# Optimization experiments

Hardware: AMD Instinct MI355X
Metric: run time of the kernel (lower is better)

Reference implementation:

```python
import jax, jax.numpy as jnp
import numpy as np

UNITS = 512
EPS = 1e-6

def setup_inputs() -> dict:
    key = jax.random.key(0)
    x = jax.random.normal(key, (262144, UNITS), dtype=jnp.float32)
    return {"x": x}

def reference(x):
    d = x.shape[1]
    # Gram matrix with diagonal jitter: [d, d]
    g = x.T @ x + jnp.eye(d, dtype=x.dtype) * EPS
    L = jnp.linalg.cholesky(g)  # lower triangular [d, d]
    # inv(L) via triangular solve (same math as tf.linalg.inv on L)
    L_inv = jax.scipy.linalg.solve_triangular(L, jnp.eye(d, dtype=x.dtype), lower=True)
    ortho_weights = L_inv.T * jnp.sqrt(jnp.float32(UNITS))
    return x @ ortho_weights
```

## Files before the change

kernel.cpp:

```cpp
#include <hip/hip_runtime.h>


#define EPSJ 1e-6f
#define SQRTD 22.627416997969522f

typedef short bf16x8 __attribute__((ext_vector_type(8)));
typedef float f32x4 __attribute__((ext_vector_type(4)));

__device__ __forceinline__ unsigned short f2bf(float f) {
  unsigned u = __float_as_uint(f);
  unsigned r = u + 0x7fffu + ((u >> 16) & 1u);
  return (unsigned short)(r >> 16);
}

__device__ __forceinline__ int swz(int row, int slot) {
  return slot ^ ((row ^ (row >> 3)) & 7);
}

__device__ __forceinline__ float wred(float s) {
  s += __shfl_xor(s, 1);  s += __shfl_xor(s, 2);  s += __shfl_xor(s, 4);
  s += __shfl_xor(s, 8);  s += __shfl_xor(s, 16); s += __shfl_xor(s, 32);
  return s;
}

#define GLOAD16(g, l)                                                         \
  __builtin_amdgcn_global_load_lds(                                           \
      (const __attribute__((address_space(1))) void*)(g),                     \
      (__attribute__((address_space(3))) void*)(l), 16, 0, 0)

__global__ void convert_bf(const float* __restrict__ X,
                           unsigned short* __restrict__ Xbf) {
  long idx = (long)blockIdx.x * blockDim.x + threadIdx.x;
  const long stride = (long)gridDim.x * blockDim.x;
  const long nch = 134217728 / 8;
  for (long i = idx; i < nch; i += stride) {
    float4 f0 = ((const float4*)X)[i * 2];
    float4 f1 = ((const float4*)X)[i * 2 + 1];
    uint4 o;
    o.x = (unsigned)f2bf(f0.x) | ((unsigned)f2bf(f0.y) << 16);
    o.y = (unsigned)f2bf(f0.z) | ((unsigned)f2bf(f0.w) << 16);
    o.z = (unsigned)f2bf(f1.x) | ((unsigned)f2bf(f1.y) << 16);
    o.w = (unsigned)f2bf(f1.z) | ((unsigned)f2bf(f1.w) << 16);
    ((uint4*)Xbf)[i] = o;
  }
}

__device__ __forceinline__ void stage_pack4(
    const unsigned short* __restrict__ src,
    unsigned short* dst, int c0, int kg) {
  uint4 r0 = *(const uint4*)src;
  uint4 r1 = *(const uint4*)(src + 512);
  uint4 r2 = *(const uint4*)(src + 1024);
  uint4 r3 = *(const uint4*)(src + 1536);
  unsigned a[4] = {r0.x, r0.y, r0.z, r0.w};
  unsigned b[4] = {r1.x, r1.y, r1.z, r1.w};
  unsigned c[4] = {r2.x, r2.y, r2.z, r2.w};
  unsigned d[4] = {r3.x, r3.y, r3.z, r3.w};
  const int khi = kg >> 1, koff = (kg & 1) * 8;
  #pragma unroll
  for (int s = 0; s < 8; ++s) {
    int wsel = s >> 1, sh = (s & 1) * 16;
    unsigned v0 = (a[wsel] >> sh) & 0xFFFFu;
    unsigned v1 = (b[wsel] >> sh) & 0xFFFFu;
    unsigned v2 = (c[wsel] >> sh) & 0xFFFFu;
    unsigned v3 = (d[wsel] >> sh) & 0xFFFFu;
    int cc = c0 + s;
    int sl = khi ^ ((cc ^ (cc >> 3)) & 7);
    *(uint2*)((char*)dst + cc * 128 + sl * 16 + koff) =
        make_uint2(v0 | (v1 << 16), v2 | (v3 << 16));
  }
}

__global__ __launch_bounds__(512, 2) void gram_bf(
    const unsigned short* __restrict__ Xbf, float* __restrict__ part,
    int nchunk) {
  __shared__ unsigned short As[256 * 64];
  __shared__ unsigned short Bs[256 * 64];
  const int b = blockIdx.x, pos = b % 3, chunk = b / 3;
  const int s0 = (int)((long)4096 * chunk / nchunk);
  const int s1 = (int)((long)4096 * (chunk + 1) / nchunk);
  const int ca = (pos == 1) ? 256 : 0;
  const int cb2 = (pos == 0) ? 0 : 256;
  const bool diag = (pos != 2);
  const int t = threadIdx.x, lane = t & 63, w = t >> 6;
  const int wr = w >> 2, wc = w & 3;

  f32x4 acc[8][4];
  const f32x4 zf = {0.f, 0.f, 0.f, 0.f};
  #pragma unroll
  for (int a = 0; a < 8; ++a)
    #pragma unroll
    for (int bb = 0; bb < 4; ++bb) acc[a][bb] = zf;

  const int c0 = (t & 31) * 8;
  const int kg = t >> 5;

  for (int ks = s0; ks < s1; ++ks) {
    long r = (long)ks * 64 + kg * 4;
    stage_pack4(Xbf + r * 512 + ca + c0, As, c0, kg);
    if (!diag) stage_pack4(Xbf + r * 512 + cb2 + c0, Bs, c0, kg);
    __syncthreads();
    const unsigned short* Bp = diag ? As : Bs;
    #pragma unroll
    for (int kk = 0; kk < 2; ++kk) {
      bf16x8 af[8], bfr[4];
      #pragma unroll
      for (int fm = 0; fm < 8; ++fm) {
        int row = wr * 128 + fm * 16 + (lane & 15);
        int slot = swz(row, kk * 4 + (lane >> 4));
        af[fm] = *(const bf16x8*)((const char*)As + row * 128 + slot * 16);
      }
      #pragma unroll
      for (int fn = 0; fn < 4; ++fn) {
        int row = wc * 64 + fn * 16 + (lane & 15);
        int slot = swz(row, kk * 4 + (lane >> 4));
        bfr[fn] = *(const bf16x8*)((const char*)Bp + row * 128 + slot * 16);
      }
      #pragma unroll
      for (int fm = 0; fm < 8; ++fm)
        #pragma unroll
        for (int fn = 0; fn < 4; ++fn)
          acc[fm][fn] = __builtin_amdgcn_mfma_f32_16x16x32_bf16(
              bfr[fn], af[fm], acc[fm][fn], 0, 0, 0);
    }
    __syncthreads();
  }
  float* out = part + (long)b * 65536;
  #pragma unroll
  for (int fm = 0; fm < 8; ++fm)
    #pragma unroll
    for (int fn = 0; fn < 4; ++fn) {
      int mi = wr * 128 + fm * 16 + (lane & 15);
      int nj = wc * 64 + fn * 16 + (lane >> 4) * 4;
      *(float4*)(out + mi * 256 + nj) = *(float4*)&acc[fm][fn];
    }
}

__global__ __launch_bounds__(512, 2) void gram_f32(
    const float* __restrict__ X, float* __restrict__ part, int nchunk) {
  __shared__ unsigned short As[256 * 64];
  __shared__ unsigned short Bs[256 * 64];
  const int b = blockIdx.x;
  const int pos = b % 3;
  const int chunk = b / 3;
  const int CR = 262144 / nchunk;
  const long r0 = (long)chunk * CR;
  const int ca = (pos == 1) ? 256 : 0;
  const int cb = (pos == 0) ? 0 : 256;
  const bool diag = (pos != 2);
  const int t = threadIdx.x, lane = t & 63, w = t >> 6;
  const int wr = w >> 2, wc = w & 3;

  f32x4 acc[8][4];
  const f32x4 zf = {0.f, 0.f, 0.f, 0.f};
  #pragma unroll
  for (int a = 0; a < 8; ++a)
    #pragma unroll
    for (int bb = 0; bb < 4; ++bb) acc[a][bb] = zf;

  const int c_oct = t & 31, msub = t >> 5;

  for (int ks = 0; ks < CR; ks += 64) {
    #pragma unroll
    for (int it = 0; it < 4; ++it) {
      int m = msub + 16 * it;
      long row = r0 + ks + m;
      const float4* sa = (const float4*)(X + row * 512 + ca + c_oct * 8);
      float4 a0 = sa[0], a1 = sa[1];
      {
        float v[8] = {a0.x, a0.y, a0.z, a0.w, a1.x, a1.y, a1.z, a1.w};
        #pragma unroll
        for (int s = 0; s < 8; ++s) {
          int c = c_oct * 8 + s;
          int off = c * 128 + ((2 * m) ^ (((c ^ (c >> 3)) & 7) << 4));
          *(unsigned short*)((char*)As + off) = f2bf(v[s]);
        }
      }
      if (!diag) {
        const float4* sb = (const float4*)(X + row * 512 + cb + c_oct * 8);
        float4 b0 = sb[0], b1 = sb[1];
        float v[8] = {b0.x, b0.y, b0.z, b0.w, b1.x, b1.y, b1.z, b1.w};
        #pragma unroll
        for (int s = 0; s < 8; ++s) {
          int c = c_oct * 8 + s;
          int off = c * 128 + ((2 * m) ^ (((c ^ (c >> 3)) & 7) << 4));
          *(unsigned short*)((char*)Bs + off) = f2bf(v[s]);
        }
      }
    }
    __syncthreads();
    const unsigned short* Bp = diag ? As : Bs;
    #pragma unroll
    for (int kk = 0; kk < 2; ++kk) {
      bf16x8 af[8], bfr[4];
      #pragma unroll
      for (int fm = 0; fm < 8; ++fm) {
        int row = wr * 128 + fm * 16 + (lane & 15);
        int slot = swz(row, kk * 4 + (lane >> 4));
        af[fm] = *(const bf16x8*)((const char*)As + row * 128 + slot * 16);
      }
      #pragma unroll
      for (int fn = 0; fn < 4; ++fn) {
        int row = wc * 64 + fn * 16 + (lane & 15);
        int slot = swz(row, kk * 4 + (lane >> 4));
        bfr[fn] = *(const bf16x8*)((const char*)Bp + row * 128 + slot * 16);
      }
      #pragma unroll
      for (int fm = 0; fm < 8; ++fm)
        #pragma unroll
        for (int fn = 0; fn < 4; ++fn)
          acc[fm][fn] = __builtin_amdgcn_mfma_f32_16x16x32_bf16(
              af[fm], bfr[fn], acc[fm][fn], 0, 0, 0);
    }
    __syncthreads();
  }
  float* out = part + (long)b * 65536;
  #pragma unroll
  for (int fm = 0; fm < 8; ++fm)
    #pragma unroll
    for (int fn = 0; fn < 4; ++fn)
      #pragma unroll
      for (int j = 0; j < 4; ++j) {
        int i  = wr * 128 + fm * 16 + (lane >> 4) * 4 + j;
        int jj = wc * 64 + fn * 16 + (lane & 15);
        out[i * 256 + jj] = acc[fm][fn][j];
      }
}

__global__ void gram_reduce(const float* __restrict__ part,
                            float* __restrict__ G, int nchunk) {
  int idx = blockIdx.x * 256 + threadIdx.x;
  int pos = idx >> 16;
  int e = idx & 65535;
  float s = 0.f;
  for (int ch = 0; ch < nchunk; ++ch)
    s += part[(long)(ch * 3 + pos) * 65536 + e];
  int i = e >> 8, j = e & 255;
  if (pos == 0) {
    G[i * 512 + j] = s;
  } else if (pos == 1) {
    G[(256 + i) * 512 + 256 + j] = s;
  } else {
    G[i * 512 + 256 + j] = s;
    G[(256 + j) * 512 + i] = s;
  }
}

__global__ __launch_bounds__(256) void chol_d64(float* __restrict__ G,
                                                float* __restrict__ Dinv,
                                                int p) {
  __shared__ float Pb[64][65];
  __shared__ float Sb[64][65];
  __shared__ float Inv[64][65];
  __shared__ float Tt[32][33];
  const int t = threadIdx.x;
  const int r0 = 64 * p;
  const int tr = (t >> 4) * 4, tc = (t & 15) * 4;

  for (int idx = t; idx < 4096; idx += 256) {
    int i = idx >> 6, j = idx & 63;
    float v = G[(long)(r0 + i) * 512 + r0 + j];
    if (i == j) v += EPSJ;
    Pb[i][j] = v;
  }
  __syncthreads();

  if (p > 0) {
    float cc[4][4] = {{0.f}};
    for (int r = 0; r < p; ++r) {
      for (int idx = t; idx < 4096; idx += 256) {
        int i = idx >> 6, j = idx & 63;
        Sb[i][j] = G[(long)(r0 + i) * 512 + 64 * r + j];
      }
      __syncthreads();
      #pragma unroll 4
      for (int k = 0; k < 64; ++k) {
        float a0 = Sb[tr][k], a1 = Sb[tr+1][k], a2 = Sb[tr+2][k], a3 = Sb[tr+3][k];
        float b0 = Sb[tc][k], b1 = Sb[tc+1][k], b2 = Sb[tc+2][k], b3 = Sb[tc+3][k];
        cc[0][0]+=a0*b0; cc[0][1]+=a0*b1; cc[0][2]+=a0*b2; cc[0][3]+=a0*b3;
        cc[1][0]+=a1*b0; cc[1][1]+=a1*b1; cc[1][2]+=a1*b2; cc[1][3]+=a1*b3;
        cc[2][0]+=a2*b0; cc[2][1]+=a2*b1; cc[2][2]+=a2*b2; cc[2][3]+=a2*b3;
        cc[3][0]+=a3*b0; cc[3][1]+=a3*b1; cc[3][2]+=a3*b2; cc[3][3]+=a3*b3;
      }
      __syncthreads();
    }
    #pragma unroll
    for (int u = 0; u < 4; ++u)
      #pragma unroll
      for (int v = 0; v < 4; ++v)
        Pb[tr + u][tc + v] -= cc[u][v];
    __syncthreads();
  }

  const int lane = t & 63, w = t >> 6;
  #pragma unroll
  for (int sp = 0; sp < 2; ++sp) {
    const int b0 = sp * 32;
    if (w == 0) {
      float rr[32];
      #pragma unroll
      for (int k = 0; k < 32; ++k)
        rr[k] = (lane < 32) ? Pb[b0 + lane][b0 + k] : 0.f;
      #pragma unroll
      for (int j = 0; j < 32; ++j) {
        float d = sqrtf(__shfl(rr[j], j));
        if (lane == j) rr[j] = d;
        else if (lane > j && lane < 32) rr[j] = rr[j] / d;
        float rj = rr[j];
        #pragma unroll
        for (int k = j + 1; k < 32; ++k) {
          float Lkj = __shfl(rj, k);
          if (lane > j && lane < 32) rr[k] -= rj * Lkj;
        }
      }
      #pragma unroll
      for (int k = 0; k < 32; ++k)
        if (lane < 32) Pb[b0 + lane][b0 + k] = rr[k];
    }
    __syncthreads();
    if (sp == 0) {
      if (t < 32) {
        int rw = 32 + t;
        float x[32];
        #pragma unroll
        for (int j = 0; j < 32; ++j) x[j] = Pb[rw][j];
        #pragma unroll
        for (int j = 0; j < 32; ++j) {
          float xj = x[j] / Pb[j][j];
          x[j] = xj;
          #pragma unroll
          for (int k2 = j + 1; k2 < 32; ++k2) x[k2] -= xj * Pb[k2][j];
        }
        #pragma unroll
        for (int j = 0; j < 32; ++j) Pb[rw][j] = x[j];
      }
      __syncthreads();
      {
        int i = 32 + (t >> 3), kb = 32 + (t & 7) * 4;
        float sv[4];
        #pragma unroll
        for (int e = 0; e < 4; ++e) sv[e] = Pb[i][kb + e];
        #pragma unroll 4
        for (int j = 0; j < 32; ++j) {
          float aij = Pb[i][j];
          #pragma unroll
          for (int e = 0; e < 4; ++e) sv[e] -= aij * Pb[kb + e][j];
        }
        #pragma unroll
        for (int e = 0; e < 4; ++e) Pb[i][kb + e] = sv[e];
      }
      __syncthreads();
    }
  }

  if (t < 64) {
    int col = t & 31, o = (t >> 5) * 32;
    float x[32];
    #pragma unroll
    for (int i = 0; i < 32; ++i) {
      float s = (i == col) ? 1.f : 0.f;
      #pragma unroll
      for (int j = 0; j < i; ++j) s -= Pb[o + i][o + j] * x[j];
      x[i] = s / Pb[o + i][o + i];
    }
    #pragma unroll
    for (int i = 0; i < 32; ++i) Inv[o + i][o + col] = x[i];
  }
  for (int idx = t; idx < 1024; idx += 256)
    Inv[idx >> 5][32 + (idx & 31)] = 0.f;
  __syncthreads();
  {
    int i = t >> 3, jb = (t & 7) * 4;
    float sv[4] = {0.f, 0.f, 0.f, 0.f};
    #pragma unroll 4
    for (int k = 0; k < 32; ++k) {
      float bik = Pb[32 + i][k];
      #pragma unroll
      for (int e = 0; e < 4; ++e) sv[e] += bik * Inv[k][jb + e];
    }
    #pragma unroll
    for (int e = 0; e < 4; ++e) Tt[i][jb + e] = sv[e];
  }
  __syncthreads();
  {
    int i = t >> 3, jb = (t & 7) * 4;
    float sv[4] = {0.f, 0.f, 0.f, 0.f};
    #pragma unroll 4
    for (int k = 0; k < 32; ++k) {
      float cik = Inv[32 + i][32 + k];
      #pragma unroll
      for (int e = 0; e < 4; ++e) sv[e] += cik * Tt[k][jb + e];
    }
    #pragma unroll
    for (int e = 0; e < 4; ++e) Inv[32 + i][jb + e] = -sv[e];
  }
  __syncthreads();
  for (int idx = t; idx < 4096; idx += 256) {
    int i = idx >> 6, j = idx & 63;
    G[(long)(r0 + i) * 512 + r0 + j] = Pb[i][j];
    Dinv[p * 4096 + idx] = Inv[i][j];
  }
}

__global__ __launch_bounds__(256) void chol_t64(float* __restrict__ G,
                                                const float* __restrict__ Dinv,
                                                int p) {
  __shared__ float SbI[64][65];
  __shared__ float SbP[64][65];
  __shared__ float Ub[64][65];
  __shared__ float Db[64][65];
  const int t = threadIdx.x;
  const long rI = 64 * (p + 1 + blockIdx.x), cP = 64 * p;
  const int tr = (t >> 4) * 4, tc = (t & 15) * 4;

  for (int idx = t; idx < 4096; idx += 256)
    Db[idx >> 6][idx & 63] = Dinv[p * 4096 + idx];

  float cc[4][4] = {{0.f}};
  for (int r = 0; r < p; ++r) {
    __syncthreads();
    for (int idx = t; idx < 4096; idx += 256) {
      int i = idx >> 6, j = idx & 63;
      SbI[i][j] = G[(rI + i) * 512 + 64 * r + j];
      SbP[i][j] = G[(cP + i) * 512 + 64 * r + j];
    }
    __syncthreads();
    #pragma unroll 4
    for (int k = 0; k < 64; ++k) {
      float a0 = SbI[tr][k], a1 = SbI[tr+1][k], a2 = SbI[tr+2][k], a3 = SbI[tr+3][k];
      float b0 = SbP[tc][k], b1 = SbP[tc+1][k], b2 = SbP[tc+2][k], b3 = SbP[tc+3][k];
      cc[0][0]+=a0*b0; cc[0][1]+=a0*b1; cc[0][2]+=a0*b2; cc[0][3]+=a0*b3;
      cc[1][0]+=a1*b0; cc[1][1]+=a1*b1; cc[1][2]+=a1*b2; cc[1][3]+=a1*b3;
      cc[2][0]+=a2*b0; cc[2][1]+=a2*b1; cc[2][2]+=a2*b2; cc[2][3]+=a2*b3;
      cc[3][0]+=a3*b0; cc[3][1]+=a3*b1; cc[3][2]+=a3*b2; cc[3][3]+=a3*b3;
    }
  }
  __syncthreads();
  #pragma unroll
  for (int u = 0; u < 4; ++u)
    #pragma unroll
    for (int v = 0; v < 4; ++v)
      Ub[tr + u][tc + v] =
          G[(rI + tr + u) * 512 + cP + tc + v] - cc[u][v];
  __syncthreads();
  float xx[4][4] = {{0.f}};
  #pragma unroll 4
  for (int k = 0; k < 64; ++k) {
    float a0 = Ub[tr][k], a1 = Ub[tr+1][k], a2 = Ub[tr+2][k], a3 = Ub[tr+3][k];
    float b0 = Db[tc][k], b1 = Db[tc+1][k], b2 = Db[tc+2][k], b3 = Db[tc+3][k];
    xx[0][0]+=a0*b0; xx[0][1]+=a0*b1; xx[0][2]+=a0*b2; xx[0][3]+=a0*b3;
    xx[1][0]+=a1*b0; xx[1][1]+=a1*b1; xx[1][2]+=a1*b2; xx[1][3]+=a1*b3;
    xx[2][0]+=a2*b0; xx[2][1]+=a2*b1; xx[2][2]+=a2*b2; xx[2][3]+=a2*b3;
    xx[3][0]+=a3*b0; xx[3][1]+=a3*b1; xx[3][2]+=a3*b2; xx[3][3]+=a3*b3;
  }
  #pragma unroll
  for (int u = 0; u < 4; ++u)
    #pragma unroll
    for (int v = 0; v < 4; ++v)
      G[(rI + tr + u) * 512 + cP + tc + v] = xx[u][v];
}

__global__ __launch_bounds__(256) void tri_assemble(
    const float* __restrict__ G, const float* __restrict__ Dinv,
    unsigned short* __restrict__ Wt) {
  __shared__ float Bsh[448 * 64];
  __shared__ float T[64 * 64];
  const int q = blockIdx.x, t = threadIdx.x;
  const int or_ = (t >> 4) * 4, oc = (t & 15) * 4;

  for (int p = q + 1; p < 8; ++p) {
    float cc[4][4] = {{0.f}};
    for (int r = q; r < p; ++r) {
      const float* Lbase = G + (long)(64 * p) * 512 + 64 * r;
      #pragma unroll 4
      for (int k = 0; k < 64; ++k) {
        float a0 = Lbase[(or_ + 0) * 512 + k];
        float a1 = Lbase[(or_ + 1) * 512 + k];
        float a2 = Lbase[(or_ + 2) * 512 + k];
        float a3 = Lbase[(or_ + 3) * 512 + k];
        float b0, b1, b2, b3;
        if (r == q) {
          const float* Bq = Dinv + q * 4096 + k * 64 + oc;
          b0 = Bq[0]; b1 = Bq[1]; b2 = Bq[2]; b3 = Bq[3];
        } else {
          const float* Br = Bsh + ((r - q - 1) * 64 + k) * 64 + oc;
          b0 = Br[0]; b1 = Br[1]; b2 = Br[2]; b3 = Br[3];
        }
        cc[0][0] += a0*b0; cc[0][1] += a0*b1; cc[0][2] += a0*b2; cc[0][3] += a0*b3;
        cc[1][0] += a1*b0; cc[1][1] += a1*b1; cc[1][2] += a1*b2; cc[1][3] += a1*b3;
        cc[2][0] += a2*b0; cc[2][1] += a2*b1; cc[2][2] += a2*b2; cc[2][3] += a2*b3;
        cc[3][0] += a3*b0; cc[3][1] += a3*b1; cc[3][2] += a3*b2; cc[3][3] += a3*b3;
      }
    }
    #pragma unroll
    for (int u = 0; u < 4; ++u)
      #pragma unroll
      for (int v = 0; v < 4; ++v)
        T[(or_ + u) * 64 + oc + v] = cc[u][v];
    __syncthreads();

    float c2[4][4] = {{0.f}};
    const float* Dp = Dinv + p * 4096;
    #pragma unroll 4
    for (int k = 0; k < 64; ++k) {
      float a0 = Dp[(or_ + 0) * 64 + k];
      float a1 = Dp[(or_ + 1) * 64 + k];
      float a2 = Dp[(or_ + 2) * 64 + k];
      float a3 = Dp[(or_ + 3) * 64 + k];
      const float* Tk = T + k * 64 + oc;
      float b0 = Tk[0], b1 = Tk[1], b2 = Tk[2], b3 = Tk[3];
      c2[0][0] += a0*b0; c2[0][1] += a0*b1; c2[0][2] += a0*b2; c2[0][3] += a0*b3;
      c2[1][0] += a1*b0; c2[1][1] += a1*b1; c2[1][2] += a1*b2; c2[1][3] += a1*b3;
      c2[2][0] += a2*b0; c2[2][1] += a2*b1; c2[2][2] += a2*b2; c2[2][3] += a2*b3;
      c2[3][0] += a3*b0; c2[3][1] += a3*b1; c2[3][2] += a3*b2; c2[3][3] += a3*b3;
    }
    #pragma unroll
    for (int u = 0; u < 4; ++u)
      #pragma unroll
      for (int v = 0; v < 4; ++v)
        Bsh[((p - q - 1) * 64 + or_ + u) * 64 + oc + v] = -c2[u][v];
    __syncthreads();
  }

  const int nr = (8 - q) * 64;
  for (int idx = t; idx < nr * 64; idx += 256) {
    int i = idx >> 6, kk = idx & 63;
    float v = (i < 64) ? Dinv[q * 4096 + i * 64 + kk]
                       : Bsh[(i - 64) * 64 + kk];
    int n = 64 * q + i;
    Wt[(long)n * 512 + 64 * q + kk] = f2bf(SQRTD * v);
  }
  for (int idx = t; idx < 64 * q * 64; idx += 256) {
    int n = idx >> 6, kk = idx & 63;
    Wt[(long)n * 512 + 64 * q + kk] = 0;
  }
}

__global__ void tri_inv(const float* __restrict__ G,
                        unsigned short* __restrict__ Wt) {
  int w = threadIdx.x >> 6, lane = threadIdx.x & 63;
  int c = blockIdx.x * 4 + w;
  float v8[8];
  #pragma unroll
  for (int q = 0; q < 8; ++q) v8[q] = 0.f;
  #pragma unroll
  for (int q = 0; q < 8; ++q) {
    for (int ii = 0; ii < 64; ++ii) {
      int i = q * 64 + ii;
      const float* Lrow = G + (long)i * 512;
      float s = 0.f;
      #pragma unroll
      for (int qq = 0; qq < 8; ++qq) {
        if (qq < q) s += v8[qq] * Lrow[qq * 64 + lane];
      }
      s += (lane < ii) ? v8[q] * Lrow[q * 64 + lane] : 0.f;
      s = wred(s);
      float xi = (((i == c) ? 1.f : 0.f) - s) / Lrow[i];
      if (lane == ii) v8[q] = xi;
    }
  }
  #pragma unroll
  for (int q = 0; q < 8; ++q) {
    int i = q * 64 + lane;
    Wt[(long)i * 512 + c] = f2bf(SQRTD * v8[q]);
  }
}

__global__ __launch_bounds__(256, 3) void ymm3(
    const unsigned short* __restrict__ Xbf,
    const unsigned short* __restrict__ Wt, float* __restrict__ Y) {
  __shared__ unsigned short As[2][128 * 64];
  const int t = threadIdx.x, lane = t & 63, w = t >> 6;
  const int id = blockIdx.x;
  const int xcd = id & 7, j = id >> 3;
  const long m0 = (long)((j >> 2) * 8 + xcd) * 128;
  const int n0 = (j & 3) * 128;
  const int wm = (w >> 1) * 64, wn = (w & 1) * 64;
  const int lrow = lane >> 3, lslot = lane & 7;
  f32x4 acc[4][4];
  const f32x4 zf = {0.f, 0.f, 0.f, 0.f};
  #pragma unroll
  for (int a = 0; a < 4; ++a)
    #pragma unroll
    for (int bq = 0; bq < 4; ++bq) acc[a][bq] = zf;

  auto stage = [&](int buf, int k0) {
    #pragma unroll
    for (int jj = 0; jj < 4; ++jj) {
      int row = (w * 4 + jj) * 8 + lrow;
      const unsigned short* sA =
          Xbf + (m0 + row) * 512 + k0 + swz(row, lslot) * 8;
      GLOAD16(sA, &As[buf][(w * 4 + jj) * 512]);
    }
  };

  stage(0, 0);
  __syncthreads();
  int cur = 0;
  #pragma unroll 1
  for (int kt = 0; kt < 8; ++kt) {
    if (kt < 7) stage(cur ^ 1, (kt + 1) * 64);
    const int k0 = kt * 64;
    bf16x8 bfr[2][4];
    #pragma unroll
    for (int kk = 0; kk < 2; ++kk)
      #pragma unroll
      for (int fn = 0; fn < 4; ++fn) {
        int n = n0 + wn + fn * 16 + (lane & 15);
        bfr[kk][fn] = *(const bf16x8*)(Wt + (long)n * 512 + k0 + kk * 32 +
                                       (lane >> 4) * 8);
      }
    #pragma unroll
    for (int kk = 0; kk < 2; ++kk) {
      bf16x8 af[4];
      #pragma unroll
      for (int fm = 0; fm < 4; ++fm) {
        int row = wm + fm * 16 + (lane & 15);
        af[fm] = *(const bf16x8*)((const char*)As[cur] + row * 128 +
                                  swz(row, kk * 4 + (lane >> 4)) * 16);
      }
      #pragma unroll
      for (int fm = 0; fm < 4; ++fm)
        #pragma unroll
        for (int fn = 0; fn < 4; ++fn)
          acc[fm][fn] = __builtin_amdgcn_mfma_f32_16x16x32_bf16(
              bfr[kk][fn], af[fm], acc[fm][fn], 0, 0, 0);
    }
    __syncthreads();
    cur ^= 1;
  }

  #pragma unroll
  for (int fm = 0; fm < 4; ++fm)
    #pragma unroll
    for (int fn = 0; fn < 4; ++fn) {
      long row = m0 + wm + fm * 16 + (lane & 15);
      int col = n0 + wn + fn * 16 + (lane >> 4) * 4;
      *(float4*)(Y + row * 512 + col) = *(float4*)&acc[fm][fn];
    }
}

__global__ __launch_bounds__(256) void ymm_v1(const float* __restrict__ X,
                                              const unsigned short* __restrict__ Wt,
                                              float* __restrict__ Y) {
  __shared__ unsigned short As[128 * 64];
  __shared__ unsigned short Bs[128 * 64];
  const int t = threadIdx.x, lane = t & 63, w = t >> 6;
  const long m0 = (long)blockIdx.x * 128;
  const int n0 = blockIdx.y * 128;
  const int wm = (w >> 1) * 64, wn = (w & 1) * 64;
  f32x4 acc[4][4];
  const f32x4 zf = {0.f, 0.f, 0.f, 0.f};
  #pragma unroll
  for (int a = 0; a < 4; ++a)
    #pragma unroll
    for (int bq = 0; bq < 4; ++bq) acc[a][bq] = zf;
  const int ko = t & 7, mrow = t >> 3;

  for (int k0 = 0; k0 < 512; k0 += 64) {
    #pragma unroll
    for (int it = 0; it < 4; ++it) {
      int m = mrow + 32 * it;
      const float4* src = (const float4*)(X + (m0 + m) * 512 + k0 + ko * 8);
      float4 f0 = src[0], f1 = src[1];
      unsigned p0 = (unsigned)f2bf(f0.x) | ((unsigned)f2bf(f0.y) << 16);
      unsigned p1 = (unsigned)f2bf(f0.z) | ((unsigned)f2bf(f0.w) << 16);
      unsigned p2 = (unsigned)f2bf(f1.x) | ((unsigned)f2bf(f1.y) << 16);
      unsigned p3 = (unsigned)f2bf(f1.z) | ((unsigned)f2bf(f1.w) << 16);
      int slot = swz(m, ko);
      *(uint4*)((char*)As + m * 128 + slot * 16) = make_uint4(p0, p1, p2, p3);
    }
    #pragma unroll
    for (int it = 0; it < 4; ++it) {
      int n = mrow + 32 * it;
      uint4 raw = *(const uint4*)(Wt + (long)(n0 + n) * 512 + k0 + ko * 8);
      int slot = swz(n, ko);
      *(uint4*)((char*)Bs + n * 128 + slot * 16) = raw;
    }
    __syncthreads();
    #pragma unroll
    for (int kk = 0; kk < 2; ++kk) {
      bf16x8 af[4], bfr[4];
      #pragma unroll
      for (int fm = 0; fm < 4; ++fm) {
        int row = wm + fm * 16 + (lane & 15);
        af[fm] = *(const bf16x8*)((const char*)As + row * 128 +
                                  swz(row, kk * 4 + (lane >> 4)) * 16);
      }
      #pragma unroll
      for (int fn = 0; fn < 4; ++fn) {
        int row = wn + fn * 16 + (lane & 15);
        bfr[fn] = *(const bf16x8*)((const char*)Bs + row * 128 +
                                   swz(row, kk * 4 + (lane >> 4)) * 16);
      }
      #pragma unroll
      for (int fm = 0; fm < 4; ++fm)
        #pragma unroll
        for (int fn = 0; fn < 4; ++fn)
          acc[fm][fn] = __builtin_amdgcn_mfma_f32_16x16x32_bf16(
              af[fm], bfr[fn], acc[fm][fn], 0, 0, 0);
    }
    __syncthreads();
  }
  #pragma unroll
  for (int fm = 0; fm < 4; ++fm)
    #pragma unroll
    for (int fn = 0; fn < 4; ++fn)
      #pragma unroll
      for (int j = 0; j < 4; ++j) {
        long row = m0 + wm + fm * 16 + (lane >> 4) * 4 + j;
        int col = n0 + wn + fn * 16 + (lane & 15);
        Y[row * 512 + col] = acc[fm][fn][j];
      }
}

static void chol_chain(float* G, float* Dinv, hipStream_t stream) {
  for (int p = 0; p < 8; ++p) {
    chol_d64<<<1, 256, 0, stream>>>(G, Dinv, p);
    if (p < 7) chol_t64<<<7 - p, 256, 0, stream>>>(G, Dinv, p);
  }
}

extern "C" void kernel_launch(void* const* d_in, const int* in_sizes, int n_in,
                              void* d_out, int out_size, void* d_ws, size_t ws_size,
                              hipStream_t stream) {
  const float* X = (const float*)d_in[0];
  float* Y = (float*)d_out;
  char* ws = (char*)d_ws;
  float* G = (float*)ws;
  unsigned short* Wt = (unsigned short*)(ws + (1 << 20));
  float* Dinv = (float*)(ws + (1 << 20) + (1 << 19));

  const int NCH_FAST = 85;
  size_t part_off = (size_t)(2 << 20);
  size_t part_bytes = (size_t)NCH_FAST * 3 * 65536 * 4;
  size_t xbf_off = part_off + part_bytes;
  size_t need = xbf_off + (size_t)134217728 * 2;

  if (ws_size >= need) {
    float* part = (float*)(ws + part_off);
    unsigned short* Xbf = (unsigned short*)(ws + xbf_off);
    convert_bf<<<2048, 256, 0, stream>>>(X, Xbf);
    gram_bf<<<3 * NCH_FAST, 512, 0, stream>>>(Xbf, part, NCH_FAST);
    gram_reduce<<<768, 256, 0, stream>>>(part, G, NCH_FAST);
    chol_chain(G, Dinv, stream);
    tri_assemble<<<8, 256, 0, stream>>>(G, Dinv, Wt);
    ymm3<<<8192, 256, 0, stream>>>(Xbf, Wt, Y);
  } else {
    float* part = (float*)(ws + part_off);
    size_t fixed = part_off;
    int nchunk = 64;
    while (nchunk > 1 && fixed + (size_t)nchunk * 3 * 65536 * 4 > ws_size)
      nchunk >>= 1;
    gram_f32<<<3 * nchunk, 512, 0, stream>>>(X, part, nchunk);
    gram_reduce<<<768, 256, 0, stream>>>(part, G, nchunk);
    chol_chain(G, Dinv, stream);
    tri_inv<<<128, 256, 0, stream>>>(G, Wt);
    ymm_v1<<<dim3(2048, 4), 256, 0, stream>>>(X, Wt, Y);
  }
}
```

Before: 1.500 ms.

## Stage weight tile in LDS and use 8-wave blocks in final GEMM

The output GEMM kernel now stages the Wt (B) tile through double-buffered shared memory alongside the X tile, instead of having each wave read B fragments directly from global memory every k-step. The block grows from 4 to 8 waves, each owning a 32x64 sub-tile with half the accumulators, and the loop is restructured to peel the final compute. This is meant to cut redundant global/L2 traffic for B and raise occupancy, at the cost of doubling LDS usage per block and more LDS reads per MFMA.

```diff
diff --git a/kernel.cpp b/kernel.cpp
--- a/kernel.cpp
+++ b/kernel.cpp
@@ -566,31 +566,59 @@
   }
 }
 
-__global__ __launch_bounds__(256, 3) void ymm3(
+__global__ __launch_bounds__(512, 4) void ymm4(
     const unsigned short* __restrict__ Xbf,
     const unsigned short* __restrict__ Wt, float* __restrict__ Y) {
   __shared__ unsigned short As[2][128 * 64];
+  __shared__ unsigned short Bs[2][128 * 64];
   const int t = threadIdx.x, lane = t & 63, w = t >> 6;
   const int id = blockIdx.x;
   const int xcd = id & 7, j = id >> 3;
   const long m0 = (long)((j >> 2) * 8 + xcd) * 128;
   const int n0 = (j & 3) * 128;
-  const int wm = (w >> 1) * 64, wn = (w & 1) * 64;
-  const int lrow = lane >> 3, lslot = lane & 7;
-  f32x4 acc[4][4];
+  const int wm = (w >> 1) * 32, wn = (w & 1) * 64;
+  f32x4 acc[2][4];
   const f32x4 zf = {0.f, 0.f, 0.f, 0.f};
   #pragma unroll
-  for (int a = 0; a < 4; ++a)
+  for (int a = 0; a < 2; ++a)
     #pragma unroll
     for (int bq = 0; bq < 4; ++bq) acc[a][bq] = zf;
 
   auto stage = [&](int buf, int k0) {
     #pragma unroll
-    for (int jj = 0; jj < 4; ++jj) {
-      int row = (w * 4 + jj) * 8 + lrow;
+    for (int h = 0; h < 2; ++h) {
+      int seg = t + h * 512;
+      int row = seg >> 3, sl = seg & 7;
       const unsigned short* sA =
-          Xbf + (m0 + row) * 512 + k0 + swz(row, lslot) * 8;
-      GLOAD16(sA, &As[buf][(w * 4 + jj) * 512]);
+          Xbf + (m0 + row) * 512 + k0 + swz(row, sl) * 8;
+      const unsigned short* sB =
+          Wt + (long)(n0 + row) * 512 + k0 + swz(row, sl) * 8;
+      GLOAD16(sA, &As[buf][seg * 8]);
+      GLOAD16(sB, &Bs[buf][seg * 8]);
+    }
+  };
+  auto compute = [&](int buf) {
+    #pragma unroll
+    for (int kk = 0; kk < 2; ++kk) {
+      bf16x8 af[2], bfr[4];
+      #pragma unroll
+      for (int fm = 0; fm < 2; ++fm) {
+        int row = wm + fm * 16 + (lane & 15);
+        af[fm] = *(const bf16x8*)((const char*)As[buf] + row * 128 +
+                                  swz(row, kk * 4 + (lane >> 4)) * 16);
+      }
+      #pragma unroll
+      for (int fn = 0; fn < 4; ++fn) {
+        int row = wn + fn * 16 + (lane & 15);
+        bfr[fn] = *(const bf16x8*)((const char*)Bs[buf] + row * 128 +
+                                   swz(row, kk * 4 + (lane >> 4)) * 16);
+      }
+      #pragma unroll
+      for (int fm = 0; fm < 2; ++fm)
+        #pragma unroll
+        for (int fn = 0; fn < 4; ++fn)
+          acc[fm][fn] = __builtin_amdgcn_mfma_f32_16x16x32_bf16(
+              bfr[fn], af[fm], acc[fm][fn], 0, 0, 0);
     }
   };
 
@@ -598,40 +626,16 @@
   __syncthreads();
   int cur = 0;
   #pragma unroll 1
-  for (int kt = 0; kt < 8; ++kt) {
-    if (kt < 7) stage(cur ^ 1, (kt + 1) * 64);
-    const int k0 = kt * 64;
-    bf16x8 bfr[2][4];
-    #pragma unroll
-    for (int kk = 0; kk < 2; ++kk)
-      #pragma unroll
-      for (int fn = 0; fn < 4; ++fn) {
-        int n = n0 + wn + fn * 16 + (lane & 15);
-        bfr[kk][fn] = *(const bf16x8*)(Wt + (long)n * 512 + k0 + kk * 32 +
-                                       (lane >> 4) * 8);
-      }
-    #pragma unroll
-    for (int kk = 0; kk < 2; ++kk) {
-      bf16x8 af[4];
-      #pragma unroll
-      for (int fm = 0; fm < 4; ++fm) {
-        int row = wm + fm * 16 + (lane & 15);
-        af[fm] = *(const bf16x8*)((const char*)As[cur] + row * 128 +
-                                  swz(row, kk * 4 + (lane >> 4)) * 16);
-      }
-      #pragma unroll
-      for (int fm = 0; fm < 4; ++fm)
-        #pragma unroll
-        for (int fn = 0; fn < 4; ++fn)
-          acc[fm][fn] = __builtin_amdgcn_mfma_f32_16x16x32_bf16(
-              bfr[kk][fn], af[fm], acc[fm][fn], 0, 0, 0);
-    }
+  for (int kt = 0; kt < 7; ++kt) {
+    stage(cur ^ 1, (kt + 1) * 64);
+    compute(cur);
     __syncthreads();
     cur ^= 1;
   }
-
-  #pragma unroll
-  for (int fm = 0; fm < 4; ++fm)
+  compute(cur);
+
+  #pragma unroll
+  for (int fm = 0; fm < 2; ++fm)
     #pragma unroll
     for (int fn = 0; fn < 4; ++fn) {
       long row = m0 + wm + fm * 16 + (lane & 15);
@@ -745,7 +749,7 @@
     gram_reduce<<<768, 256, 0, stream>>>(part, G, NCH_FAST);
     chol_chain(G, Dinv, stream);
     tri_assemble<<<8, 256, 0, stream>>>(G, Dinv, Wt);
-    ymm3<<<8192, 256, 0, stream>>>(Xbf, Wt, Y);
+    ymm4<<<8192, 512, 0, stream>>>(Xbf, Wt, Y);
   } else {
     float* part = (float*)(ws + part_off);
     size_t fixed = part_off;
```

Result: faster. 1.413 ms (-5.8%).
